# Kernel optimization log

Measured on AMD Instinct MI355X. Metric: run time of the kernel, lower is better.

## Reference

```python
import jax, jax.numpy as jnp
import numpy as np

N_NODES = 100000
N_EDGES = 1600000
IN_DIM = 128
HEADS = 8
STATE_DIM = 16   # per-head hidden
OUT_DIM = 8      # per-head output
NEG_SLOPE = 0.2


def _gat_conv(x, src, dst, W, a_src, a_dst, b, num_nodes, heads, d):
    # x: [N, F_in]; W: [F_in, heads*d]; a_src/a_dst: [heads, d]; b: [heads*d]
    h = (x @ W).reshape(num_nodes, heads, d)                # [N,H,D]
    s_src = jnp.einsum('nhd,hd->nh', h, a_src)              # [N,H]
    s_dst = jnp.einsum('nhd,hd->nh', h, a_dst)              # [N,H]
    e = jax.nn.leaky_relu(s_src[src] + s_dst[dst], NEG_SLOPE)   # [E,H]
    # segment softmax over edges sharing the same destination node
    m = jax.ops.segment_max(e, dst, num_segments=num_nodes)     # [N,H]
    m = jnp.where(jnp.isfinite(m), m, jnp.zeros_like(m))
    ex = jnp.exp(e - m[dst])                                    # [E,H]
    denom = jax.ops.segment_sum(ex, dst, num_segments=num_nodes)
    alpha = ex / (denom[dst] + 1e-16)                           # [E,H]
    # weighted scatter-aggregate of source features
    out = jax.ops.segment_sum(h[src] * alpha[:, :, None], dst, num_segments=num_nodes)
    return out.reshape(num_nodes, heads * d) + b


def setup_inputs() -> dict:
    key = jax.random.key(0)
    ks = jax.random.split(key, 12)
    x = jax.random.normal(ks[0], (N_NODES, IN_DIM), dtype=jnp.float32)
    edge_index = jax.random.randint(ks[1], (2, N_EDGES), 0, N_NODES, dtype=jnp.int64)
    s1 = 1.0 / np.sqrt(IN_DIM)
    s2 = 1.0 / np.sqrt(HEADS * STATE_DIM)
    W1 = jax.random.normal(ks[2], (IN_DIM, HEADS * STATE_DIM), dtype=jnp.float32) * s1
    a1_src = jax.random.normal(ks[3], (HEADS, STATE_DIM), dtype=jnp.float32) * s2
    a1_dst = jax.random.normal(ks[4], (HEADS, STATE_DIM), dtype=jnp.float32) * s2
    b1 = jnp.zeros((HEADS * STATE_DIM,), dtype=jnp.float32)
    W2 = jax.random.normal(ks[5], (HEADS * STATE_DIM, HEADS * OUT_DIM), dtype=jnp.float32) * s2
    a2_src = jax.random.normal(ks[6], (HEADS, OUT_DIM), dtype=jnp.float32) * s2
    a2_dst = jax.random.normal(ks[7], (HEADS, OUT_DIM), dtype=jnp.float32) * s2
    b2 = jnp.zeros((HEADS * OUT_DIM,), dtype=jnp.float32)
    return {"x": x, "edge_index": edge_index, "W1": W1, "a1_src": a1_src,
            "a1_dst": a1_dst, "b1": b1, "W2": W2, "a2_src": a2_src,
            "a2_dst": a2_dst, "b2": b2}


def reference(x, edge_index, W1, a1_src, a1_dst, b1, W2, a2_src, a2_dst, b2):
    # PyG GATConv adds self-loops by default
    loops = jnp.arange(N_NODES, dtype=edge_index.dtype)
    src = jnp.concatenate([edge_index[0], loops])
    dst = jnp.concatenate([edge_index[1], loops])
    h = _gat_conv(x, src, dst, W1, a1_src, a1_dst, b1, N_NODES, HEADS, STATE_DIM)
    h = jax.nn.relu(h)  # dropout is identity at eval
    out = _gat_conv(h, src, dst, W2, a2_src, a2_dst, b2, N_NODES, HEADS, OUT_DIM)
    return out  # [N, HEADS*OUT_DIM]
```

## Files before the change

kernel.cpp:

```cpp
#include <hip/hip_runtime.h>
#include <hip/hip_fp16.h>
#include <math.h>

#define N_NODES 100000
#define N_EDGES 1600000
#define IN_DIM 128
#define HEADS 8
#define D1 16
#define D2 8
#define NEG_SLOPE 0.2f

#define NBKT ((N_NODES + 255) / 256)
#define PART_CHUNK 4096
#define BCAP 6144

typedef _Float16 f16x8 __attribute__((ext_vector_type(8)));
typedef float    f32x4 __attribute__((ext_vector_type(4)));

struct __align__(16) half8 { __half2 a, b, c, d; };

__device__ __forceinline__ f16x8 load_cvt8(const float* p) {
    float4 v0 = *(const float4*)p, v1 = *(const float4*)(p + 4);
    f16x8 r;
    r[0] = (_Float16)v0.x; r[1] = (_Float16)v0.y;
    r[2] = (_Float16)v0.z; r[3] = (_Float16)v0.w;
    r[4] = (_Float16)v1.x; r[5] = (_Float16)v1.y;
    r[6] = (_Float16)v1.z; r[7] = (_Float16)v1.w;
    return r;
}

template<int CTRL>
__device__ __forceinline__ float dpp_add(float x) {
    int y = __builtin_amdgcn_update_dpp(0, __builtin_bit_cast(int, x),
                                        CTRL, 0xF, 0xF, true);
    return x + __builtin_bit_cast(float, y);
}

template<int OUTC, int D, bool XF32>
__global__ __launch_bounds__(256)
void gemm_mfma_kernel(const void* __restrict__ Ain, const __half* __restrict__ Bt,
                      __half* __restrict__ C,
                      const float* __restrict__ a_s, const float* __restrict__ a_d,
                      float* __restrict__ s_src, float* __restrict__ s_dst,
                      int n_rows) {
    constexpr int K = 128;
    constexpr int NT = OUTC / 16;
    int wid  = threadIdx.x >> 6;
    int lane = threadIdx.x & 63;
    int row0 = blockIdx.x * 64 + wid * 16;
    int lr   = lane & 15;
    int ks   = (lane >> 4) * 8;

    int arow = row0 + lr;
    arow = arow < n_rows ? arow : n_rows - 1;

    f16x8 a0, a1, a2, a3;
    if constexpr (XF32) {
        const float* ap = (const float*)Ain + (long)arow * K + ks;
        a0 = load_cvt8(ap);
        a1 = load_cvt8(ap + 32);
        a2 = load_cvt8(ap + 64);
        a3 = load_cvt8(ap + 96);
    } else {
        const __half* ap = (const __half*)Ain + (long)arow * K + ks;
        a0 = *(const f16x8*)(ap);
        a1 = *(const f16x8*)(ap + 32);
        a2 = *(const f16x8*)(ap + 64);
        a3 = *(const f16x8*)(ap + 96);
    }

    f32x4 acc[NT];
#pragma unroll
    for (int j = 0; j < NT; ++j) acc[j] = (f32x4)(0.f);

#pragma unroll
    for (int j = 0; j < NT; ++j) {
        const __half* bp = Bt + (long)(j * 16 + lr) * K + ks;
        f16x8 b0 = *(const f16x8*)(bp);
        f16x8 b1 = *(const f16x8*)(bp + 32);
        f16x8 b2 = *(const f16x8*)(bp + 64);
        f16x8 b3 = *(const f16x8*)(bp + 96);
        acc[j] = __builtin_amdgcn_mfma_f32_16x16x32_f16(a0, b0, acc[j], 0, 0, 0);
        acc[j] = __builtin_amdgcn_mfma_f32_16x16x32_f16(a1, b1, acc[j], 0, 0, 0);
        acc[j] = __builtin_amdgcn_mfma_f32_16x16x32_f16(a2, b2, acc[j], 0, 0, 0);
        acc[j] = __builtin_amdgcn_mfma_f32_16x16x32_f16(a3, b3, acc[j], 0, 0, 0);
    }

    float asv[NT], adv[NT];
#pragma unroll
    for (int j = 0; j < NT; ++j) {
        asv[j] = a_s[j * 16 + lr];
        adv[j] = a_d[j * 16 + lr];
    }

    int rbase = row0 + (lane >> 4) * 4;
#pragma unroll
    for (int r = 0; r < 4; ++r) {
        int rr = rbase + r;
        bool valid = rr < n_rows;

        if (valid) {
            __half* cp = C + (long)rr * OUTC + lr;
#pragma unroll
            for (int j = 0; j < NT; ++j)
                cp[j * 16] = __float2half(acc[j][r]);
        }

        float ps[NT], pd[NT];
#pragma unroll
        for (int j = 0; j < NT; ++j) {
            ps[j] = acc[j][r] * asv[j];
            pd[j] = acc[j][r] * adv[j];
        }
        if constexpr (D == 16) {
#pragma unroll
            for (int j = 0; j < NT; ++j) {
                ps[j] = dpp_add<0x118>(ps[j]); ps[j] = dpp_add<0x114>(ps[j]);
                ps[j] = dpp_add<0x112>(ps[j]); ps[j] = dpp_add<0x111>(ps[j]);
                pd[j] = dpp_add<0x118>(pd[j]); pd[j] = dpp_add<0x114>(pd[j]);
                pd[j] = dpp_add<0x112>(pd[j]); pd[j] = dpp_add<0x111>(pd[j]);
            }
            if (valid && lr == 15) {
                float* sp = s_src + rr * 8;
                float* dp = s_dst + rr * 8;
                *(float4*)(sp)     = make_float4(ps[0], ps[1], ps[2], ps[3]);
                *(float4*)(sp + 4) = make_float4(ps[4], ps[5], ps[6], ps[7]);
                *(float4*)(dp)     = make_float4(pd[0], pd[1], pd[2], pd[3]);
                *(float4*)(dp + 4) = make_float4(pd[4], pd[5], pd[6], pd[7]);
            }
        } else {
#pragma unroll
            for (int j = 0; j < NT; ++j) {
                ps[j] = dpp_add<0x114>(ps[j]); ps[j] = dpp_add<0x112>(ps[j]);
                ps[j] = dpp_add<0x111>(ps[j]);
                pd[j] = dpp_add<0x114>(pd[j]); pd[j] = dpp_add<0x112>(pd[j]);
                pd[j] = dpp_add<0x111>(pd[j]);
            }
            if (valid && lr == 7) {
#pragma unroll
                for (int j = 0; j < NT; ++j) {
                    s_src[rr * 8 + 2 * j] = ps[j];
                    s_dst[rr * 8 + 2 * j] = pd[j];
                }
            }
            if (valid && lr == 15) {
#pragma unroll
                for (int j = 0; j < NT; ++j) {
                    s_src[rr * 8 + 2 * j + 1] = ps[j];
                    s_dst[rr * 8 + 2 * j + 1] = pd[j];
                }
            }
        }
    }
}

__global__ __launch_bounds__(256)
void convert_w_kernel(const float* __restrict__ W1, const float* __restrict__ W2,
                      __half* __restrict__ Wt1, __half* __restrict__ Wt2,
                      int* __restrict__ bcursor) {
    int idx = blockIdx.x * 256 + threadIdx.x;
    if (idx < NBKT) bcursor[idx] = 0;
    if (idx < 128 * 128) {
        int k = idx / 128, j = idx % 128;
        Wt1[(long)j * 128 + k] = __float2half(W1[idx]);
    } else {
        int i = idx - 128 * 128;
        if (i < 128 * 64) {
            int k = i / 64, j = i % 64;
            Wt2[(long)j * 128 + k] = __float2half(W2[i]);
        }
    }
}

__global__ __launch_bounds__(256)
void partition_kernel(const int* __restrict__ src, const int* __restrict__ dst,
                      int* __restrict__ bcursor, int2* __restrict__ bpairs) {
    __shared__ int hist[NBKT];
    for (int i = threadIdx.x; i < NBKT; i += 256) hist[i] = 0;
    __syncthreads();
    int e0 = blockIdx.x * PART_CHUNK;
    int e1 = e0 + PART_CHUNK < N_EDGES ? e0 + PART_CHUNK : N_EDGES;
    for (int e = e0 + threadIdx.x; e < e1; e += 256)
        atomicAdd(&hist[dst[e] >> 8], 1);
    __syncthreads();
    for (int i = threadIdx.x; i < NBKT; i += 256) {
        int c = hist[i];
        if (c) {
            int r = atomicAdd(&bcursor[i], c);
            hist[i] = i * BCAP + (r < BCAP ? r : BCAP);
        }
    }
    __syncthreads();
    for (int e = e0 + threadIdx.x; e < e1; e += 256) {
        int d = dst[e];
        int bkt = d >> 8;
        int pos = atomicAdd(&hist[bkt], 1);
        if (pos < (bkt + 1) * BCAP)
            bpairs[pos] = make_int2(src[e], d);
    }
}

__global__ __launch_bounds__(256)
void localcsr_kernel(const int* __restrict__ bcursor, const int2* __restrict__ bpairs,
                     int* __restrict__ row_start, int* __restrict__ row_end,
                     int* __restrict__ eidx) {
    __shared__ int cnt[256];
    __shared__ int sh[256];
    __shared__ int cur[256];
    int b = blockIdx.x;
    int tid = threadIdx.x;
    int n0 = b << 8;
    int m0 = b * BCAP;
    int count = bcursor[b];
    int m1 = m0 + (count < BCAP ? count : BCAP);
    cnt[tid] = 0;
    __syncthreads();
    for (int k = m0 + tid; k < m1; k += 256)
        atomicAdd(&cnt[bpairs[k].y & 255], 1);
    __syncthreads();
    int c = cnt[tid];
    sh[tid] = c;
    __syncthreads();
    int run = c;
    for (int off = 1; off < 256; off <<= 1) {
        int add = (tid >= off) ? sh[tid - off] : 0;
        __syncthreads();
        run += add;
        sh[tid] = run;
        __syncthreads();
    }
    int excl = run - c;
    cur[tid] = m0 + excl;
    if (n0 + tid < N_NODES) {
        row_start[n0 + tid] = m0 + excl;
        row_end[n0 + tid]   = m0 + excl + c;
    }
    __syncthreads();
    for (int k = m0 + tid; k < m1; k += 256) {
        int2 p = bpairs[k];
        int pos = atomicAdd(&cur[p.y & 255], 1);
        eidx[pos] = p.x;
    }
}

template<int D, bool RELU, typename OT>
__global__ __launch_bounds__(256)
void aggregate_wave_kernel(const int* __restrict__ rs, const int* __restrict__ re,
                           const int* __restrict__ eidx,
                           const __half* __restrict__ h,
                           const float* __restrict__ ssrc, const float* __restrict__ sdst,
                           const float* __restrict__ bias, OT* __restrict__ out) {
    constexpr int F = HEADS * D;
    constexpr int EPL = F / 64;
    int lane = threadIdx.x & 63;
    int node = blockIdx.x * (256 / 64) + (threadIdx.x >> 6);
    node = __builtin_amdgcn_readfirstlane(node);
    if (node >= N_NODES) return;
    int hd = lane >> 3;
    int esl = lane & 7;

    float sdv = sdst[node * HEADS + hd];
    float sc0 = ssrc[node * HEADS + hd] + sdv;
    float w0 = __expf(sc0 > 0.f ? sc0 : NEG_SLOPE * sc0);
    float wsum = w0;

    float accx, accy = 0.f;
    if constexpr (EPL == 2) {
        float2 v = __half22float2(*(const __half2*)(h + (long)node * F + lane * 2));
        accx = w0 * v.x; accy = w0 * v.y;
    } else {
        accx = w0 * __half2float(h[(long)node * F + lane]);
    }

    int e0 = rs[node], e1 = re[node];
    int e1m1 = e1 - 1;

    for (int e = e0; e < e1; e += 8) {
        int idx = e + esl;
        int ci = idx < e1m1 ? idx : e1m1;
        int s_mine = eidx[ci];
        float sc = ssrc[s_mine * HEADS + hd] + sdv;
        float w_mine = __expf(sc > 0.f ? sc : NEG_SLOPE * sc);
        w_mine = (idx < e1) ? w_mine : 0.f;

        int grp = lane & 56;
        if constexpr (EPL == 2) {
#pragma unroll
            for (int i = 0; i < 8; ++i) {
                float wi = __shfl(w_mine, grp + i, 64);
                int   si = __shfl(s_mine, grp + i, 64);
                wsum += wi;
                float2 v = __half22float2(*(const __half2*)(h + (long)si * F + lane * 2));
                accx = fmaf(wi, v.x, accx);
                accy = fmaf(wi, v.y, accy);
            }
        } else {
#pragma unroll
            for (int i = 0; i < 8; ++i) {
                float wi = __shfl(w_mine, grp + i, 64);
                int   si = __shfl(s_mine, grp + i, 64);
                wsum += wi;
                accx = fmaf(wi, __half2float(h[(long)si * F + lane]), accx);
            }
        }
    }

    float inv = 1.f / (wsum + 1e-16f);
    if constexpr (EPL == 2) {
        float2 b = *(const float2*)(bias + lane * 2);
        float ox = accx * inv + b.x;
        float oy = accy * inv + b.y;
        if (RELU) { ox = fmaxf(ox, 0.f); oy = fmaxf(oy, 0.f); }
        if constexpr (sizeof(OT) == 2) {
            *(__half2*)((__half*)out + (long)node * F + lane * 2) = __floats2half2_rn(ox, oy);
        } else {
            *(float2*)((float*)out + (long)node * F + lane * 2) = make_float2(ox, oy);
        }
    } else {
        float o = accx * inv + bias[lane];
        if (RELU) o = fmaxf(o, 0.f);
        if constexpr (sizeof(OT) == 2) {
            ((__half*)out)[(long)node * F + lane] = __float2half(o);
        } else {
            ((float*)out)[(long)node * F + lane] = o;
        }
    }
}

extern "C" void kernel_launch(void* const* d_in, const int* in_sizes, int n_in,
                              void* d_out, int out_size, void* d_ws, size_t ws_size,
                              hipStream_t stream) {
    const float* x   = (const float*)d_in[0];
    const int*   ei  = (const int*)d_in[1];
    const float* W1  = (const float*)d_in[2];
    const float* a1s = (const float*)d_in[3];
    const float* a1d = (const float*)d_in[4];
    const float* b1  = (const float*)d_in[5];
    const float* W2  = (const float*)d_in[6];
    const float* a2s = (const float*)d_in[7];
    const float* a2d = (const float*)d_in[8];
    const float* b2  = (const float*)d_in[9];
    float* out = (float*)d_out;

    const int* src = ei;
    const int* dst = ei + N_EDGES;

    float* ws = (float*)d_ws;
    float* bufA = ws;
    float* bufB = bufA + (size_t)N_NODES * 128;
    float* ssrc = bufB + (size_t)N_NODES * 128;
    float* sdst = ssrc + (size_t)N_NODES * HEADS;
    int* counts    = (int*)(sdst + (size_t)N_NODES * HEADS);
    int* row_start = counts + N_NODES;
    int* row_end   = row_start + N_NODES + 1;

    int* bcursor = counts + 1024;
    __half* Wt1  = (__half*)(counts + 2048);
    __half* Wt2  = (__half*)(counts + 2048 + 8192);
    int2* bpairs  = (int2*)bufB;
    __half* h1out = (__half*)bufB;
    int* eidx = (int*)((char*)bufA + (size_t)32 * 1024 * 1024);

    __half* hbuf = (__half*)bufA;

    convert_w_kernel<<<(128 * 128 + 128 * 64 + 255) / 256, 256, 0, stream>>>(
        W1, W2, Wt1, Wt2, bcursor);
    partition_kernel<<<(N_EDGES + PART_CHUNK - 1) / PART_CHUNK, 256, 0, stream>>>(
        src, dst, bcursor, bpairs);
    localcsr_kernel<<<NBKT, 256, 0, stream>>>(bcursor, bpairs, row_start, row_end, eidx);

    gemm_mfma_kernel<128, D1, true><<<(N_NODES + 63) / 64, 256, 0, stream>>>(
        x, Wt1, hbuf, a1s, a1d, ssrc, sdst, N_NODES);
    aggregate_wave_kernel<D1, true, __half><<<(N_NODES + 3) / 4, 256, 0, stream>>>(
        row_start, row_end, eidx, hbuf, ssrc, sdst, b1, h1out);

    gemm_mfma_kernel<64, D2, false><<<(N_NODES + 63) / 64, 256, 0, stream>>>(
        h1out, Wt2, hbuf, a2s, a2d, ssrc, sdst, N_NODES);
    aggregate_wave_kernel<D2, false, float><<<(N_NODES + 3) / 4, 256, 0, stream>>>(
        row_start, row_end, eidx, hbuf, ssrc, sdst, b2, out);
}
```

Before: 344.2 us.

## Fuse local CSR build with first GEMM launch and register-cache partition edges

Merges the per-bucket local CSR construction and the layer-1 MFMA GEMM into one launch, with the block index picking which role each block plays. The two independent stages can then overlap on the GPU and one launch gap disappears. The partition kernel now loads each thread's src/dst edges into registers once instead of reading dst twice and src separately. Risks are higher register and LDS pressure in the fused kernel from the union of both roles, which can lower occupancy for the GEMM blocks.

```diff
diff --git a/kernel.cpp b/kernel.cpp
--- a/kernel.cpp
+++ b/kernel.cpp
@@ -13,6 +13,7 @@
 #define NBKT ((N_NODES + 255) / 256)
 #define PART_CHUNK 4096
 #define BCAP 6144
+#define GEMM1_BLOCKS ((N_NODES + 63) / 64)
 
 typedef _Float16 f16x8 __attribute__((ext_vector_type(8)));
 typedef float    f32x4 __attribute__((ext_vector_type(4)));
@@ -37,17 +38,19 @@
 }
 
 template<int OUTC, int D, bool XF32>
-__global__ __launch_bounds__(256)
-void gemm_mfma_kernel(const void* __restrict__ Ain, const __half* __restrict__ Bt,
-                      __half* __restrict__ C,
-                      const float* __restrict__ a_s, const float* __restrict__ a_d,
-                      float* __restrict__ s_src, float* __restrict__ s_dst,
-                      int n_rows) {
+__device__ __forceinline__ void gemm_body(int gb, const void* __restrict__ Ain,
+                                          const __half* __restrict__ Bt,
+                                          __half* __restrict__ C,
+                                          const float* __restrict__ a_s,
+                                          const float* __restrict__ a_d,
+                                          float* __restrict__ s_src,
+                                          float* __restrict__ s_dst,
+                                          int n_rows) {
     constexpr int K = 128;
     constexpr int NT = OUTC / 16;
     int wid  = threadIdx.x >> 6;
     int lane = threadIdx.x & 63;
-    int row0 = blockIdx.x * 64 + wid * 16;
+    int row0 = gb * 64 + wid * 16;
     int lr   = lane & 15;
     int ks   = (lane >> 4) * 8;
 
@@ -175,13 +178,22 @@
 __global__ __launch_bounds__(256)
 void partition_kernel(const int* __restrict__ src, const int* __restrict__ dst,
                       int* __restrict__ bcursor, int2* __restrict__ bpairs) {
+    constexpr int EPT = PART_CHUNK / 256;
     __shared__ int hist[NBKT];
     for (int i = threadIdx.x; i < NBKT; i += 256) hist[i] = 0;
     __syncthreads();
     int e0 = blockIdx.x * PART_CHUNK;
-    int e1 = e0 + PART_CHUNK < N_EDGES ? e0 + PART_CHUNK : N_EDGES;
-    for (int e = e0 + threadIdx.x; e < e1; e += 256)
-        atomicAdd(&hist[dst[e] >> 8], 1);
+    int sv[EPT], dv[EPT];
+#pragma unroll
+    for (int j = 0; j < EPT; ++j) {
+        int e = e0 + j * 256 + threadIdx.x;
+        bool ok = e < N_EDGES;
+        dv[j] = ok ? dst[e] : -1;
+        sv[j] = ok ? src[e] : 0;
+    }
+#pragma unroll
+    for (int j = 0; j < EPT; ++j)
+        if (dv[j] >= 0) atomicAdd(&hist[dv[j] >> 8], 1);
     __syncthreads();
     for (int i = threadIdx.x; i < NBKT; i += 256) {
         int c = hist[i];
@@ -191,19 +203,31 @@
         }
     }
     __syncthreads();
-    for (int e = e0 + threadIdx.x; e < e1; e += 256) {
-        int d = dst[e];
-        int bkt = d >> 8;
-        int pos = atomicAdd(&hist[bkt], 1);
-        if (pos < (bkt + 1) * BCAP)
-            bpairs[pos] = make_int2(src[e], d);
+#pragma unroll
+    for (int j = 0; j < EPT; ++j) {
+        if (dv[j] >= 0) {
+            int bkt = dv[j] >> 8;
+            int pos = atomicAdd(&hist[bkt], 1);
+            if (pos < (bkt + 1) * BCAP)
+                bpairs[pos] = make_int2(sv[j], dv[j]);
+        }
     }
 }
 
 __global__ __launch_bounds__(256)
-void localcsr_kernel(const int* __restrict__ bcursor, const int2* __restrict__ bpairs,
-                     int* __restrict__ row_start, int* __restrict__ row_end,
-                     int* __restrict__ eidx) {
+void localcsr_gemm1_kernel(const int* __restrict__ bcursor,
+                           const int2* __restrict__ bpairs,
+                           int* __restrict__ row_start, int* __restrict__ row_end,
+                           int* __restrict__ eidx,
+                           const float* __restrict__ x, const __half* __restrict__ Wt1,
+                           __half* __restrict__ C,
+                           const float* __restrict__ a_s, const float* __restrict__ a_d,
+                           float* __restrict__ s_src, float* __restrict__ s_dst) {
+    if (blockIdx.x >= NBKT) {
+        gemm_body<128, D1, true>(blockIdx.x - NBKT, x, Wt1, C,
+                                 a_s, a_d, s_src, s_dst, N_NODES);
+        return;
+    }
     __shared__ int cnt[256];
     __shared__ int sh[256];
     __shared__ int cur[256];
@@ -241,6 +265,14 @@
         int pos = atomicAdd(&cur[p.y & 255], 1);
         eidx[pos] = p.x;
     }
+}
+
+__global__ __launch_bounds__(256)
+void gemm2_kernel(const __half* __restrict__ A, const __half* __restrict__ Bt,
+                  __half* __restrict__ C,
+                  const float* __restrict__ a_s, const float* __restrict__ a_d,
+                  float* __restrict__ s_src, float* __restrict__ s_dst) {
+    gemm_body<64, D2, false>(blockIdx.x, A, Bt, C, a_s, a_d, s_src, s_dst, N_NODES);
 }
 
 template<int D, bool RELU, typename OT>
@@ -367,15 +399,13 @@
         W1, W2, Wt1, Wt2, bcursor);
     partition_kernel<<<(N_EDGES + PART_CHUNK - 1) / PART_CHUNK, 256, 0, stream>>>(
         src, dst, bcursor, bpairs);
-    localcsr_kernel<<<NBKT, 256, 0, stream>>>(bcursor, bpairs, row_start, row_end, eidx);
-
-    gemm_mfma_kernel<128, D1, true><<<(N_NODES + 63) / 64, 256, 0, stream>>>(
-        x, Wt1, hbuf, a1s, a1d, ssrc, sdst, N_NODES);
+    localcsr_gemm1_kernel<<<NBKT + GEMM1_BLOCKS, 256, 0, stream>>>(
+        bcursor, bpairs, row_start, row_end, eidx,
+        x, Wt1, hbuf, a1s, a1d, ssrc, sdst);
     aggregate_wave_kernel<D1, true, __half><<<(N_NODES + 3) / 4, 256, 0, stream>>>(
         row_start, row_end, eidx, hbuf, ssrc, sdst, b1, h1out);
-
-    gemm_mfma_kernel<64, D2, false><<<(N_NODES + 63) / 64, 256, 0, stream>>>(
-        h1out, Wt2, hbuf, a2s, a2d, ssrc, sdst, N_NODES);
+    gemm2_kernel<<<GEMM1_BLOCKS, 256, 0, stream>>>(
+        h1out, Wt2, hbuf, a2s, a2d, ssrc, sdst);
     aggregate_wave_kernel<D2, false, float><<<(N_NODES + 3) / 4, 256, 0, stream>>>(
         row_start, row_end, eidx, hbuf, ssrc, sdst, b2, out);
 }
```

Result: faster. 331.9 us (-3.6%).
